# Kernel tuning notes

Measured on AMD Instinct MI355X. Metric: run time of the kernel, lower is better.

The kernel has to match this reference:

```python
import jax, jax.numpy as jnp
import numpy as np

N_EMBED = 2048
N_HEAD = 16
HEAD_DIM = N_EMBED // N_HEAD
ROPE_BASE = 500000


def _rope_cos_sin(T, dim, base):
    # torchtune RotaryPositionalEmbeddings: interleaved pairs
    inv_freq = 1.0 / (base ** (jnp.arange(0, dim, 2, dtype=jnp.float32) / dim))  # [dim/2]
    pos = jnp.arange(T, dtype=jnp.float32)
    ang = pos[:, None] * inv_freq[None, :]  # [T, dim/2]
    return jnp.cos(ang), jnp.sin(ang)


def _apply_rope(x, cos, sin):
    # x: [B, T, H, D]; cos/sin: [T, D/2] -> broadcast [1, T, 1, D/2]
    c = cos[None, :, None, :]
    s = sin[None, :, None, :]
    x1 = x[..., 0::2]
    x2 = x[..., 1::2]
    r1 = x1 * c - x2 * s
    r2 = x2 * c + x1 * s
    return jnp.stack([r1, r2], axis=-1).reshape(x.shape)


def setup_inputs() -> dict:
    key = jax.random.key(0)
    k1, k2, k3 = jax.random.split(key, 3)
    B, T, C = 4, 2048, N_EMBED
    x = jax.random.normal(k1, (B, T, C), dtype=jnp.float32)
    Wqkv = jax.random.normal(k2, (C, 3 * C), dtype=jnp.float32) * 0.02
    Wproj = jax.random.normal(k3, (C, C), dtype=jnp.float32) * 0.02
    return {"x": x, "Wqkv": Wqkv, "Wproj": Wproj}


def reference(x, Wqkv, Wproj):
    B, T, C = x.shape
    H, D = N_HEAD, HEAD_DIM
    qkv = x @ Wqkv  # [B, T, 3C]
    q, k, v = jnp.split(qkv, 3, axis=2)
    q = q.reshape(B, T, H, D)
    k = k.reshape(B, T, H, D)
    v = v.reshape(B, T, H, D)
    cos, sin = _rope_cos_sin(T, D, ROPE_BASE)
    q = _apply_rope(q, cos, sin)
    k = _apply_rope(k, cos, sin)
    scale = 1.0 / jnp.sqrt(jnp.float32(D))
    # causal SDPA: scores [B, H, T, T]
    scores = jnp.einsum('bqhd,bkhd->bhqk', q, k) * scale
    mask = jnp.tril(jnp.ones((T, T), dtype=bool))
    scores = jnp.where(mask[None, None, :, :], scores, jnp.float32(-1e30))
    attn = jax.nn.softmax(scores, axis=-1)
    y = jnp.einsum('bhqk,bkhd->bqhd', attn, v).reshape(B, T, C)
    return y @ Wproj
```

## Files before the change

### kernel.cpp

```cpp
#include <hip/hip_runtime.h>
#include <math.h>

#define NB 4
#define TT 2048
#define CC 2048
#define HH 16
#define DD 128
#define N3 6144
#define MM 8192
#define BH 64

typedef short bf8 __attribute__((ext_vector_type(8)));
typedef float f32x4 __attribute__((ext_vector_type(4)));
typedef unsigned short u16x8 __attribute__((ext_vector_type(8)));
typedef unsigned short u16;

constexpr float SCALE_QK  = 0.08838834764831843f;
constexpr float NEG_ALPHA = -0.20503692777194262f;

__device__ __forceinline__ u16 f2bf(float x) {
    unsigned int u = __float_as_uint(x);
    u += 0x7fffu + ((u >> 16) & 1u);
    return (u16)(u >> 16);
}
__device__ __forceinline__ float bf2f(u16 h) { return __uint_as_float(((unsigned int)h) << 16); }

__device__ __forceinline__ void gl_lds16(const u16* g, u16* l) {
    __builtin_amdgcn_global_load_lds(reinterpret_cast<const unsigned int*>(g),
                                     reinterpret_cast<unsigned int*>(l), 16, 0, 0);
}
__device__ __forceinline__ f32x4 MFMA(bf8 a, bf8 b, f32x4 c) {
    return __builtin_amdgcn_mfma_f32_16x16x32_bf16(a, b, c, 0, 0, 0);
}

#define BAR()    __builtin_amdgcn_s_barrier()
#define SCHED0() __builtin_amdgcn_sched_barrier(0)
#define WAIT_LGKM0() do { asm volatile("s_waitcnt lgkmcnt(0)" ::: "memory"); SCHED0(); } while (0)
#define WAIT_VM8()   do { asm volatile("s_waitcnt vmcnt(8)"   ::: "memory"); SCHED0(); } while (0)
#define WAIT_VM4()   do { asm volatile("s_waitcnt vmcnt(4)"   ::: "memory"); SCHED0(); } while (0)
#define WAIT_VM0()   do { asm volatile("s_waitcnt vmcnt(0)"   ::: "memory"); SCHED0(); } while (0)

__global__ void rope_tab_k(float* __restrict__ tab) {
    int t = blockIdx.x, p = threadIdx.x;
    float inv = expf((float)p * NEG_ALPHA);
    float s, c;
    sincosf((float)t * inv, &s, &c);
    tab[(t * 64 + p) * 2]     = c;
    tab[(t * 64 + p) * 2 + 1] = s;
}

__global__ __launch_bounds__(256) void split_x_k(const float* __restrict__ X,
                                                 u16* __restrict__ H, u16* __restrict__ L) {
    size_t base = ((size_t)blockIdx.x * 256 + threadIdx.x) * 16;
    #pragma unroll
    for (int g = 0; g < 2; ++g) {
        u16x8 hv, lv;
        #pragma unroll
        for (int j = 0; j < 8; j += 4) {
            float4 a = *(const float4*)(X + base + g * 8 + j);
            float xs[4] = {a.x, a.y, a.z, a.w};
            #pragma unroll
            for (int q = 0; q < 4; ++q) {
                u16 h = f2bf(xs[q]);
                hv[j + q] = h;
                lv[j + q] = f2bf(xs[q] - bf2f(h));
            }
        }
        *(u16x8*)&H[base + g * 8] = hv;
        *(u16x8*)&L[base + g * 8] = lv;
    }
}

__global__ __launch_bounds__(256) void splitT_h(const float* __restrict__ W,
                                                u16* __restrict__ OH,
                                                int Kd, int Nd) {
    __shared__ float tile[64][68];
    int k0 = blockIdx.x * 64, n0 = blockIdx.y * 64;
    {
        int r = threadIdx.x >> 2, cg = threadIdx.x & 3;
        const float* src = W + (size_t)(k0 + r) * Nd + n0 + cg * 16;
        #pragma unroll
        for (int j = 0; j < 4; ++j)
            *(float4*)&tile[r][cg * 16 + j * 4] = *(const float4*)(src + j * 4);
    }
    __syncthreads();
    int nl = threadIdx.x >> 2, kg = threadIdx.x & 3;
    u16x8 hv[2];
    #pragma unroll
    for (int j = 0; j < 16; ++j)
        hv[j >> 3][j & 7] = f2bf(tile[kg * 16 + j][nl]);
    size_t off = (size_t)(n0 + nl) * Kd + k0 + kg * 16;
    *(u16x8*)&OH[off]     = hv[0];
    *(u16x8*)&OH[off + 8] = hv[1];
}

template<int MODE>
__global__ __launch_bounds__(512, 2) void gemm8p(
    const u16* __restrict__ Ahp, const u16* __restrict__ Alp,
    const u16* __restrict__ Bhp,
    u16* __restrict__ Qh, u16* __restrict__ Ql,
    u16* __restrict__ Kbo, u16* __restrict__ Vto,
    const float* __restrict__ tab, float* __restrict__ Out)
{
    __shared__ u16 SM[66048];

    const int tid = threadIdx.x;
    const int w = tid >> 6, ln = tid & 63;
    const int lo4 = ln & 15, hi4 = ln >> 4;
    const int wr = w >> 2, wc = w & 3;
    const int m0 = blockIdx.x * 256, n0 = blockIdx.y * 256;
    const int NKT = 64;

    f32x4 acc[8][4];
    #pragma unroll
    for (int i = 0; i < 8; ++i)
        #pragma unroll
        for (int j = 0; j < 4; ++j) acc[i][j] = (f32x4){0.f, 0.f, 0.f, 0.f};

    auto stage = [&](int s) {
        if (s >= 4 * NKT) return;
        const int tau = s >> 2, j = s & 3;
        const int c2 = tau & 1, op = j >> 1, hf = j & 1;
        const int tdiv = tau >> 5, tmod = tau & 31;
        const u16* plane;
        int row0;
        if (op == 0) { plane = tdiv ? Alp : Ahp; row0 = m0 + hf * 128; }
        else         { plane = Bhp;              row0 = n0 + hf * 128; }
        u16* dst = SM + (op ? 32768 : 0) + (c2 * 2 + hf) * 8192;
        #pragma unroll
        for (int i = 0; i < 2; ++i) {
            int L = i * 8192 + tid * 16;
            int r = L >> 7;
            int c = (L >> 4) & 7;
            int cs = c ^ (r & 7);
            gl_lds16(plane + (size_t)(row0 + r) * 2048 + tmod * 64 + cs * 8,
                     dst + (L >> 1));
        }
    };

    #pragma unroll
    for (int s = 0; s < 6; ++s) stage(s);
    WAIT_VM4();
    BAR();

    bf8 a03[4][2], a47[4][2], b01[2][2], b23[2][2];
    const int brow0 = (wc & 1) * 64;

    for (int t = 0; t < NKT; ++t) {
        const int c2 = t & 1;
        const u16* Ab = SM + (c2 * 2 + wr) * 8192;
        const u16* Bb = SM + 32768 + (c2 * 2 + (wc >> 1)) * 8192;

        #pragma unroll
        for (int mf = 0; mf < 4; ++mf) {
            int rr = mf * 16 + lo4, s7 = rr & 7;
            a03[mf][0] = *(const bf8*)&Ab[rr * 64 + ((hi4 ^ s7)) * 8];
            a03[mf][1] = *(const bf8*)&Ab[rr * 64 + (((4 + hi4) ^ s7)) * 8];
        }
        #pragma unroll
        for (int nf = 0; nf < 2; ++nf) {
            int rr = brow0 + nf * 16 + lo4, s7 = rr & 7;
            b01[nf][0] = *(const bf8*)&Bb[rr * 64 + ((hi4 ^ s7)) * 8];
            b01[nf][1] = *(const bf8*)&Bb[rr * 64 + (((4 + hi4) ^ s7)) * 8];
        }
        stage(4 * t + 6);
        BAR(); WAIT_LGKM0();
        __builtin_amdgcn_s_setprio(1);
        #pragma unroll
        for (int mf = 0; mf < 4; ++mf)
            #pragma unroll
            for (int nf = 0; nf < 2; ++nf) {
                acc[mf][nf] = MFMA(a03[mf][0], b01[nf][0], acc[mf][nf]);
                acc[mf][nf] = MFMA(a03[mf][1], b01[nf][1], acc[mf][nf]);
            }
        __builtin_amdgcn_s_setprio(0);
        BAR();

        #pragma unroll
        for (int mf = 0; mf < 4; ++mf) {
            int rr = 64 + mf * 16 + lo4, s7 = rr & 7;
            a47[mf][0] = *(const bf8*)&Ab[rr * 64 + ((hi4 ^ s7)) * 8];
            a47[mf][1] = *(const bf8*)&Ab[rr * 64 + (((4 + hi4) ^ s7)) * 8];
        }
        stage(4 * t + 7);
        BAR(); WAIT_LGKM0();
        __builtin_amdgcn_s_setprio(1);
        #pragma unroll
        for (int mf = 0; mf < 4; ++mf)
            #pragma unroll
            for (int nf = 0; nf < 2; ++nf) {
                acc[4 + mf][nf] = MFMA(a47[mf][0], b01[nf][0], acc[4 + mf][nf]);
                acc[4 + mf][nf] = MFMA(a47[mf][1], b01[nf][1], acc[4 + mf][nf]);
            }
        __builtin_amdgcn_s_setprio(0);
        BAR();

        #pragma unroll
        for (int nf = 0; nf < 2; ++nf) {
            int rr = brow0 + 32 + nf * 16 + lo4, s7 = rr & 7;
            b23[nf][0] = *(const bf8*)&Bb[rr * 64 + ((hi4 ^ s7)) * 8];
            b23[nf][1] = *(const bf8*)&Bb[rr * 64 + (((4 + hi4) ^ s7)) * 8];
        }
        stage(4 * t + 8);
        BAR(); WAIT_LGKM0();
        __builtin_amdgcn_s_setprio(1);
        #pragma unroll
        for (int mf = 0; mf < 4; ++mf)
            #pragma unroll
            for (int nf = 0; nf < 2; ++nf) {
                acc[mf][2 + nf] = MFMA(a03[mf][0], b23[nf][0], acc[mf][2 + nf]);
                acc[mf][2 + nf] = MFMA(a03[mf][1], b23[nf][1], acc[mf][2 + nf]);
            }
        __builtin_amdgcn_s_setprio(0);
        BAR();

        stage(4 * t + 9);
        BAR();
        __builtin_amdgcn_s_setprio(1);
        #pragma unroll
        for (int mf = 0; mf < 4; ++mf)
            #pragma unroll
            for (int nf = 0; nf < 2; ++nf) {
                acc[4 + mf][2 + nf] = MFMA(a47[mf][0], b23[nf][0], acc[4 + mf][2 + nf]);
                acc[4 + mf][2 + nf] = MFMA(a47[mf][1], b23[nf][1], acc[4 + mf][2 + nf]);
            }
        __builtin_amdgcn_s_setprio(0);
        if (t < NKT - 2)       { WAIT_VM4(); }
        else if (t == NKT - 2) { WAIT_VM0(); }
        BAR();
    }

    if (MODE == 1) {
        #pragma unroll
        for (int mf = 0; mf < 8; ++mf)
            #pragma unroll
            for (int r = 0; r < 4; ++r) {
                int m = m0 + wr * 128 + mf * 16 + hi4 * 4 + r;
                float* rowp = Out + (size_t)m * CC + n0 + wc * 64;
                #pragma unroll
                for (int nf = 0; nf < 4; ++nf)
                    rowp[nf * 16 + lo4] = acc[mf][nf][r];
            }
        return;
    }

    const int sec = n0 >> 11;
    const int hh0 = (n0 >> 7) & 15;
    if (sec < 2) {
        #pragma unroll
        for (int mf = 0; mf < 8; ++mf)
            #pragma unroll
            for (int r = 0; r < 4; ++r) {
                int m = m0 + wr * 128 + mf * 16 + hi4 * 4 + r;
                int t = m & 2047, b = m >> 11;
                #pragma unroll
                for (int nf = 0; nf < 4; ++nf) {
                    int nl = wc * 64 + nf * 16 + lo4;
                    int h = hh0 + (nl >> 7), d = nl & 127;
                    float v = acc[mf][nf][r];
                    float o = __shfl_xor(v, 1);
                    const float2 cs2 = *(const float2*)&tab[(((size_t)t << 6) + (d >> 1)) * 2];
                    float rv = (ln & 1) ? (v * cs2.x + o * cs2.y)
                                        : (v * cs2.x - o * cs2.y);
                    size_t off = (((size_t)(b * HH + h)) * TT + t) * DD + d;
                    if (sec == 0) {
                        rv *= SCALE_QK;
                        u16 hv = f2bf(rv);
                        Qh[off] = hv;
                        Ql[off] = f2bf(rv - bf2f(hv));
                    } else {
                        Kbo[off] = f2bf(rv);
                    }
                }
            }
    } else {
        BAR();
        #pragma unroll
        for (int mf = 0; mf < 8; ++mf)
            #pragma unroll
            for (int r = 0; r < 4; ++r) {
                int tl = wr * 128 + mf * 16 + hi4 * 4 + r;
                #pragma unroll
                for (int nf = 0; nf < 4; ++nf) {
                    int nl = wc * 64 + nf * 16 + lo4;
                    SM[tl * 258 + nl] = f2bf(acc[mf][nf][r]);
                }
            }
        BAR();
        int nl = tid >> 1, th = tid & 1;
        int head = hh0 + (nl >> 7), d = nl & 127;
        int b = m0 >> 11, t0 = m0 & 2047;
        size_t base = (((size_t)(b * HH + head)) * DD + d) * TT + t0 + th * 128;
        #pragma unroll
        for (int g = 0; g < 16; ++g) {
            u16x8 vv;
            #pragma unroll
            for (int j = 0; j < 8; ++j) vv[j] = SM[(th * 128 + g * 8 + j) * 258 + nl];
            *(u16x8*)&Vto[base + g * 8] = vv;
        }
    }
}

__global__ __launch_bounds__(256, 2) void attn128(
    const u16* __restrict__ Qhp, const u16* __restrict__ Qlp,
    const u16* __restrict__ Kb,  const u16* __restrict__ Vt,
    u16* __restrict__ Yh, u16* __restrict__ Yl)
{
    __shared__ u16 SM[40960];

    const int tid = threadIdx.x;
    const int w = tid >> 6, ln = tid & 63;
    const int lo4 = ln & 15, hi4 = ln >> 4;
    const int bx = blockIdx.x;
    const int qt = (bx & 1) ? (15 - (bx >> 1)) : (bx >> 1);
    const int bh = blockIdx.y;
    const int q0 = qt * 128;
    const int last = 2 * qt + 1;

    const size_t qoff = ((size_t)bh * TT + q0) * DD;
    #pragma unroll
    for (int i = 0; i < 8; ++i) {
        int L = i * 4096 + tid * 16;
        int r = L >> 8, c = (L >> 4) & 15;
        int cs = c ^ (r & 7);
        gl_lds16(Qhp + qoff + r * DD + cs * 8, &SM[L >> 1]);
        gl_lds16(Qlp + qoff + r * DD + cs * 8, &SM[16384 + (L >> 1)]);
    }
    WAIT_VM0();
    BAR();
    bf8 qh[2][4], ql[2][4];
    #pragma unroll
    for (int mf = 0; mf < 2; ++mf) {
        int rq = w * 32 + mf * 16 + lo4, s7 = rq & 7;
        #pragma unroll
        for (int ks = 0; ks < 4; ++ks) {
            int ch = (ks * 4 + hi4) ^ s7;
            qh[mf][ks] = *(const bf8*)&SM[rq * 128 + ch * 8];
            ql[mf][ks] = *(const bf8*)&SM[16384 + rq * 128 + ch * 8];
        }
    }
    WAIT_LGKM0();
    BAR();

    auto stageKV = [&](int kt2, int buf) {
        const size_t koff = ((size_t)bh * TT + kt2 * 64) * DD;
        u16* kd = &SM[buf * 8192];
        #pragma unroll
        for (int i = 0; i < 4; ++i) {
            int L = i * 4096 + tid * 16;
            int r = L >> 8, c = (L >> 4) & 15, cs = c ^ (r & 7);
            gl_lds16(Kb + koff + r * DD + cs * 8, kd + (L >> 1));
        }
        const size_t voff = (size_t)bh * DD * TT + (size_t)kt2 * 64;
        u16* vd = &SM[16384 + buf * 8192];
        #pragma unroll
        for (int i = 0; i < 4; ++i) {
            int L = i * 4096 + tid * 16;
            int r = L >> 7, c = (L >> 4) & 7, cs = c ^ (r & 7);
            gl_lds16(Vt + voff + (size_t)r * TT + cs * 8, vd + (L >> 1));
        }
    };
    stageKV(0, 0);

    f32x4 O[2][8];
    #pragma unroll
    for (int mf = 0; mf < 2; ++mf)
        #pragma unroll
        for (int i = 0; i < 8; ++i) O[mf][i] = (f32x4){0.f, 0.f, 0.f, 0.f};
    float m_r[2][4], l_r[2][4];
    #pragma unroll
    for (int mf = 0; mf < 2; ++mf)
        #pragma unroll
        for (int r = 0; r < 4; ++r) { m_r[mf][r] = -1e30f; l_r[mf][r] = 0.f; }

    for (int kt = 0; kt <= last; ++kt) {
        const int cur = kt & 1;
        if (kt < last) { stageKV(kt + 1, cur ^ 1); WAIT_VM8(); }
        else           { WAIT_VM0(); }
        BAR();
        const u16* Kcur = &SM[cur * 8192];
        const u16* Vcur = &SM[16384 + cur * 8192];

        f32x4 sf[2][4];
        #pragma unroll
        for (int nf = 0; nf < 4; ++nf) {
            f32x4 s0 = (f32x4){0.f, 0.f, 0.f, 0.f};
            f32x4 s1 = (f32x4){0.f, 0.f, 0.f, 0.f};
            int kr = nf * 16 + lo4, s7 = kr & 7;
            #pragma unroll
            for (int ks = 0; ks < 4; ++ks) {
                bf8 bb = *(const bf8*)&Kcur[kr * 128 + ((ks * 4 + hi4) ^ s7) * 8];
                s0 = MFMA(qh[0][ks], bb, s0);
                s0 = MFMA(ql[0][ks], bb, s0);
                s1 = MFMA(qh[1][ks], bb, s1);
                s1 = MFMA(ql[1][ks], bb, s1);
            }
            sf[0][nf] = s0; sf[1][nf] = s1;
        }
        if (kt >= 2 * qt) {
            #pragma unroll
            for (int mf = 0; mf < 2; ++mf)
                #pragma unroll
                for (int nf = 0; nf < 4; ++nf)
                    #pragma unroll
                    for (int r = 0; r < 4; ++r) {
                        int kg = kt * 64 + nf * 16 + lo4;
                        int qg = q0 + w * 32 + mf * 16 + hi4 * 4 + r;
                        if (kg > qg) sf[mf][nf][r] = -1e30f;
                    }
        }

        #pragma unroll
        for (int mf = 0; mf < 2; ++mf) {
            float mx[4];
            #pragma unroll
            for (int r = 0; r < 4; ++r) {
                float m2 = fmaxf(fmaxf(sf[mf][0][r], sf[mf][1][r]),
                                 fmaxf(sf[mf][2][r], sf[mf][3][r]));
                m2 = fmaxf(m2, __shfl_xor(m2, 1));
                m2 = fmaxf(m2, __shfl_xor(m2, 2));
                m2 = fmaxf(m2, __shfl_xor(m2, 4));
                m2 = fmaxf(m2, __shfl_xor(m2, 8));
                mx[r] = m2;
            }
            float al[4] = {1.f, 1.f, 1.f, 1.f};
            bool grow = (mx[0] > m_r[mf][0]) || (mx[1] > m_r[mf][1]) ||
                        (mx[2] > m_r[mf][2]) || (mx[3] > m_r[mf][3]);
            if (__any(grow)) {
                #pragma unroll
                for (int r = 0; r < 4; ++r) {
                    float mn = fmaxf(m_r[mf][r], mx[r]);
                    al[r] = __expf(m_r[mf][r] - mn);
                    m_r[mf][r] = mn;
                }
                #pragma unroll
                for (int nf2 = 0; nf2 < 8; ++nf2)
                    #pragma unroll
                    for (int r = 0; r < 4; ++r) O[mf][nf2][r] *= al[r];
            }
            #pragma unroll
            for (int r = 0; r < 4; ++r) {
                float rs = 0.f;
                #pragma unroll
                for (int nf = 0; nf < 4; ++nf) {
                    float p = __expf(sf[mf][nf][r] - m_r[mf][r]);
                    sf[mf][nf][r] = p;
                    rs += p;
                }
                rs += __shfl_xor(rs, 1);
                rs += __shfl_xor(rs, 2);
                rs += __shfl_xor(rs, 4);
                rs += __shfl_xor(rs, 8);
                l_r[mf][r] = l_r[mf][r] * al[r] + rs;
            }
        }

        u16* pw = &SM[32768 + w * 2048];
        #pragma unroll
        for (int mf = 0; mf < 2; ++mf)
            #pragma unroll
            for (int r = 0; r < 4; ++r) {
                int row = mf * 16 + hi4 * 4 + r;
                int sw = (row & 7) << 3;
                #pragma unroll
                for (int nf = 0; nf < 4; ++nf)
                    pw[row * 64 + ((nf * 16 + lo4) ^ sw)] = f2bf(sf[mf][nf][r]);
            }
        bf8 pa[2][2];
        #pragma unroll
        for (int mf = 0; mf < 2; ++mf) {
            int rp = mf * 16 + lo4, s3 = rp & 7;
            pa[mf][0] = *(const bf8*)&pw[rp * 64 + ((hi4 ^ s3) * 8)];
            pa[mf][1] = *(const bf8*)&pw[rp * 64 + (((4 + hi4) ^ s3) * 8)];
        }
        #pragma unroll
        for (int nf2 = 0; nf2 < 8; ++nf2) {
            int vr = nf2 * 16 + lo4, s7 = vr & 7;
            #pragma unroll
            for (int ks = 0; ks < 2; ++ks) {
                bf8 vb = *(const bf8*)&Vcur[vr * 64 + ((ks * 4 + hi4) ^ s7) * 8];
                O[0][nf2] = MFMA(pa[0][ks], vb, O[0][nf2]);
                O[1][nf2] = MFMA(pa[1][ks], vb, O[1][nf2]);
            }
        }
        BAR();
    }

    const int b = bh >> 4, h = bh & 15;
    #pragma unroll
    for (int mf = 0; mf < 2; ++mf)
        #pragma unroll
        for (int r = 0; r < 4; ++r) {
            float inv = 1.0f / l_r[mf][r];
            int t = q0 + w * 32 + mf * 16 + hi4 * 4 + r;
            size_t rowo = ((size_t)(b * TT + t)) * CC + h * DD;
            #pragma unroll
            for (int nf2 = 0; nf2 < 8; ++nf2) {
                float val = O[mf][nf2][r] * inv;
                u16 hv = f2bf(val);
                Yh[rowo + nf2 * 16 + lo4] = hv;
                Yl[rowo + nf2 * 16 + lo4] = f2bf(val - bf2f(hv));
            }
        }
}

extern "C" void kernel_launch(void* const* d_in, const int* in_sizes, int n_in,
                              void* d_out, int out_size, void* d_ws, size_t ws_size,
                              hipStream_t stream)
{
    const float* X     = (const float*)d_in[0];
    const float* Wqkv  = (const float*)d_in[1];
    const float* Wproj = (const float*)d_in[2];

    char* W = (char*)d_ws;
    float* tab = (float*)W;
    u16* Wqh = (u16*)(W + (1u << 20));
    u16* Wph = Wqh + 12582912;
    u16* Xh  = Wph + 4194304;
    u16* Xl  = Xh + 16777216;
    u16* Kb  = Xl + 16777216;
    u16* Vt  = Kb + 16777216;

    u16* Qh = (u16*)d_out;
    u16* Ql = Qh + 16777216;

    u16* Yh = Xh;
    u16* Yl = Xl;

    rope_tab_k<<<dim3(2048), 64, 0, stream>>>(tab);
    split_x_k<<<dim3(4096), 256, 0, stream>>>(X, Xh, Xl);
    splitT_h<<<dim3(32, 96), 256, 0, stream>>>(Wqkv, Wqh, 2048, 6144);
    splitT_h<<<dim3(32, 32), 256, 0, stream>>>(Wproj, Wph, 2048, 2048);

    gemm8p<0><<<dim3(32, 24), 512, 0, stream>>>(Xh, Xl, Wqh,
                                                Qh, Ql, Kb, Vt, tab, nullptr);
    attn128<<<dim3(16, 64), 256, 0, stream>>>(Qh, Ql, Kb, Vt, Yh, Yl);
    gemm8p<1><<<dim3(32, 8), 512, 0, stream>>>(Yh, Yl, Wph,
                                               nullptr, nullptr, nullptr, nullptr,
                                               nullptr, (float*)d_out);
}
```

Measured before the change: 1.017 ms.

## Switch GEMMs to 32x32x16 MFMA tiles and remap block order for XCD locality

Replaces the 16x16x32 bf16 MFMA fragments in the QKV and projection GEMMs with 32x32x16 MFMA, so each wave issues fewer, larger matrix instructions and does fewer LDS fragment reads per output. The epilogues are rewritten for the 32x32 accumulator register layout. The grid is also flattened to 1D with a block-id swizzle, (bid&7)*N + bid>>3, which groups neighbouring tiles onto the same XCD to improve L2 reuse. The cost is more accumulator registers per fragment and a different epilogue access pattern.

```diff
diff --git a/kernel.cpp b/kernel.cpp
--- a/kernel.cpp
+++ b/kernel.cpp
@@ -12,6 +12,7 @@
 
 typedef short bf8 __attribute__((ext_vector_type(8)));
 typedef float f32x4 __attribute__((ext_vector_type(4)));
+typedef float f32x16 __attribute__((ext_vector_type(16)));
 typedef unsigned short u16x8 __attribute__((ext_vector_type(8)));
 typedef unsigned short u16;
 
@@ -31,6 +32,9 @@
 }
 __device__ __forceinline__ f32x4 MFMA(bf8 a, bf8 b, f32x4 c) {
     return __builtin_amdgcn_mfma_f32_16x16x32_bf16(a, b, c, 0, 0, 0);
+}
+__device__ __forceinline__ f32x16 MFMA32(bf8 a, bf8 b, f32x16 c) {
+    return __builtin_amdgcn_mfma_f32_32x32x16_bf16(a, b, c, 0, 0, 0);
 }
 
 #define BAR()    __builtin_amdgcn_s_barrier()
@@ -95,27 +99,30 @@
 }
 
 template<int MODE>
-__global__ __launch_bounds__(512, 2) void gemm8p(
+__device__ __forceinline__ void gemm32_body(
     const u16* __restrict__ Ahp, const u16* __restrict__ Alp,
     const u16* __restrict__ Bhp,
     u16* __restrict__ Qh, u16* __restrict__ Ql,
     u16* __restrict__ Kbo, u16* __restrict__ Vto,
-    const float* __restrict__ tab, float* __restrict__ Out)
+    const float* __restrict__ tab, float* __restrict__ Out,
+    int bx, int by)
 {
     __shared__ u16 SM[66048];
 
     const int tid = threadIdx.x;
     const int w = tid >> 6, ln = tid & 63;
-    const int lo4 = ln & 15, hi4 = ln >> 4;
+    const int l31 = ln & 31, l5 = ln >> 5;
     const int wr = w >> 2, wc = w & 3;
-    const int m0 = blockIdx.x * 256, n0 = blockIdx.y * 256;
+    const int m0 = bx * 256, n0 = by * 256;
     const int NKT = 64;
 
-    f32x4 acc[8][4];
-    #pragma unroll
-    for (int i = 0; i < 8; ++i)
-        #pragma unroll
-        for (int j = 0; j < 4; ++j) acc[i][j] = (f32x4){0.f, 0.f, 0.f, 0.f};
+    f32x16 acc[4][2];
+    #pragma unroll
+    for (int i = 0; i < 4; ++i)
+        #pragma unroll
+        for (int j = 0; j < 2; ++j)
+            #pragma unroll
+            for (int r = 0; r < 16; ++r) acc[i][j][r] = 0.f;
 
     auto stage = [&](int s) {
         if (s >= 4 * NKT) return;
@@ -143,7 +150,7 @@
     WAIT_VM4();
     BAR();
 
-    bf8 a03[4][2], a47[4][2], b01[2][2], b23[2][2];
+    bf8 aF[4][4], bF[2][4];
     const int brow0 = (wc & 1) * 64;
 
     for (int t = 0; t < NKT; ++t) {
@@ -152,65 +159,61 @@
         const u16* Bb = SM + 32768 + (c2 * 2 + (wc >> 1)) * 8192;
 
         #pragma unroll
-        for (int mf = 0; mf < 4; ++mf) {
-            int rr = mf * 16 + lo4, s7 = rr & 7;
-            a03[mf][0] = *(const bf8*)&Ab[rr * 64 + ((hi4 ^ s7)) * 8];
-            a03[mf][1] = *(const bf8*)&Ab[rr * 64 + (((4 + hi4) ^ s7)) * 8];
-        }
-        #pragma unroll
-        for (int nf = 0; nf < 2; ++nf) {
-            int rr = brow0 + nf * 16 + lo4, s7 = rr & 7;
-            b01[nf][0] = *(const bf8*)&Bb[rr * 64 + ((hi4 ^ s7)) * 8];
-            b01[nf][1] = *(const bf8*)&Bb[rr * 64 + (((4 + hi4) ^ s7)) * 8];
+        for (int mt = 0; mt < 2; ++mt) {
+            int rl = mt * 32 + l31, s7 = rl & 7;
+            #pragma unroll
+            for (int ks = 0; ks < 4; ++ks)
+                aF[mt][ks] = *(const bf8*)&Ab[rl * 64 + (((ks * 2 + l5) ^ s7)) * 8];
+        }
+        {
+            int rl = brow0 + l31, s7 = rl & 7;
+            #pragma unroll
+            for (int ks = 0; ks < 4; ++ks)
+                bF[0][ks] = *(const bf8*)&Bb[rl * 64 + (((ks * 2 + l5) ^ s7)) * 8];
         }
         stage(4 * t + 6);
         BAR(); WAIT_LGKM0();
         __builtin_amdgcn_s_setprio(1);
         #pragma unroll
-        for (int mf = 0; mf < 4; ++mf)
-            #pragma unroll
-            for (int nf = 0; nf < 2; ++nf) {
-                acc[mf][nf] = MFMA(a03[mf][0], b01[nf][0], acc[mf][nf]);
-                acc[mf][nf] = MFMA(a03[mf][1], b01[nf][1], acc[mf][nf]);
-            }
+        for (int mt = 0; mt < 2; ++mt)
+            #pragma unroll
+            for (int ks = 0; ks < 4; ++ks)
+                acc[mt][0] = MFMA32(aF[mt][ks], bF[0][ks], acc[mt][0]);
         __builtin_amdgcn_s_setprio(0);
         BAR();
 
         #pragma unroll
-        for (int mf = 0; mf < 4; ++mf) {
-            int rr = 64 + mf * 16 + lo4, s7 = rr & 7;
-            a47[mf][0] = *(const bf8*)&Ab[rr * 64 + ((hi4 ^ s7)) * 8];
-            a47[mf][1] = *(const bf8*)&Ab[rr * 64 + (((4 + hi4) ^ s7)) * 8];
+        for (int mt = 2; mt < 4; ++mt) {
+            int rl = mt * 32 + l31, s7 = rl & 7;
+            #pragma unroll
+            for (int ks = 0; ks < 4; ++ks)
+                aF[mt][ks] = *(const bf8*)&Ab[rl * 64 + (((ks * 2 + l5) ^ s7)) * 8];
         }
         stage(4 * t + 7);
         BAR(); WAIT_LGKM0();
         __builtin_amdgcn_s_setprio(1);
         #pragma unroll
-        for (int mf = 0; mf < 4; ++mf)
-            #pragma unroll
-            for (int nf = 0; nf < 2; ++nf) {
-                acc[4 + mf][nf] = MFMA(a47[mf][0], b01[nf][0], acc[4 + mf][nf]);
-                acc[4 + mf][nf] = MFMA(a47[mf][1], b01[nf][1], acc[4 + mf][nf]);
-            }
+        for (int mt = 2; mt < 4; ++mt)
+            #pragma unroll
+            for (int ks = 0; ks < 4; ++ks)
+                acc[mt][0] = MFMA32(aF[mt][ks], bF[0][ks], acc[mt][0]);
         __builtin_amdgcn_s_setprio(0);
         BAR();
 
-        #pragma unroll
-        for (int nf = 0; nf < 2; ++nf) {
-            int rr = brow0 + 32 + nf * 16 + lo4, s7 = rr & 7;
-            b23[nf][0] = *(const bf8*)&Bb[rr * 64 + ((hi4 ^ s7)) * 8];
-            b23[nf][1] = *(const bf8*)&Bb[rr * 64 + (((4 + hi4) ^ s7)) * 8];
+        {
+            int rl = brow0 + 32 + l31, s7 = rl & 7;
+            #pragma unroll
+            for (int ks = 0; ks < 4; ++ks)
+                bF[1][ks] = *(const bf8*)&Bb[rl * 64 + (((ks * 2 + l5) ^ s7)) * 8];
         }
         stage(4 * t + 8);
         BAR(); WAIT_LGKM0();
         __builtin_amdgcn_s_setprio(1);
         #pragma unroll
-        for (int mf = 0; mf < 4; ++mf)
-            #pragma unroll
-            for (int nf = 0; nf < 2; ++nf) {
-                acc[mf][2 + nf] = MFMA(a03[mf][0], b23[nf][0], acc[mf][2 + nf]);
-                acc[mf][2 + nf] = MFMA(a03[mf][1], b23[nf][1], acc[mf][2 + nf]);
-            }
+        for (int mt = 0; mt < 2; ++mt)
+            #pragma unroll
+            for (int ks = 0; ks < 4; ++ks)
+                acc[mt][1] = MFMA32(aF[mt][ks], bF[1][ks], acc[mt][1]);
         __builtin_amdgcn_s_setprio(0);
         BAR();
 
@@ -218,28 +221,28 @@
         BAR();
         __builtin_amdgcn_s_setprio(1);
         #pragma unroll
-        for (int mf = 0; mf < 4; ++mf)
-            #pragma unroll
-            for (int nf = 0; nf < 2; ++nf) {
-                acc[4 + mf][2 + nf] = MFMA(a47[mf][0], b23[nf][0], acc[4 + mf][2 + nf]);
-                acc[4 + mf][2 + nf] = MFMA(a47[mf][1], b23[nf][1], acc[4 + mf][2 + nf]);
-            }
+        for (int mt = 2; mt < 4; ++mt)
+            #pragma unroll
+            for (int ks = 0; ks < 4; ++ks)
+                acc[mt][1] = MFMA32(aF[mt][ks], bF[1][ks], acc[mt][1]);
         __builtin_amdgcn_s_setprio(0);
         if (t < NKT - 2)       { WAIT_VM4(); }
         else if (t == NKT - 2) { WAIT_VM0(); }
         BAR();
     }
 
+    const int colbase = wc * 64 + l31;
     if (MODE == 1) {
         #pragma unroll
-        for (int mf = 0; mf < 8; ++mf)
-            #pragma unroll
-            for (int r = 0; r < 4; ++r) {
-                int m = m0 + wr * 128 + mf * 16 + hi4 * 4 + r;
-                float* rowp = Out + (size_t)m * CC + n0 + wc * 64;
-                #pragma unroll
-                for (int nf = 0; nf < 4; ++nf)
-                    rowp[nf * 16 + lo4] = acc[mf][nf][r];
+        for (int mt = 0; mt < 4; ++mt)
+            #pragma unroll
+            for (int nt = 0; nt < 2; ++nt) {
+                int n = n0 + colbase + nt * 32;
+                #pragma unroll
+                for (int reg = 0; reg < 16; ++reg) {
+                    int m = m0 + wr * 128 + mt * 32 + (reg & 3) + 8 * (reg >> 2) + 4 * l5;
+                    Out[(size_t)m * CC + n] = acc[mt][nt][reg];
+                }
             }
         return;
     }
@@ -248,16 +251,16 @@
     const int hh0 = (n0 >> 7) & 15;
     if (sec < 2) {
         #pragma unroll
-        for (int mf = 0; mf < 8; ++mf)
-            #pragma unroll
-            for (int r = 0; r < 4; ++r) {
-                int m = m0 + wr * 128 + mf * 16 + hi4 * 4 + r;
-                int t = m & 2047, b = m >> 11;
-                #pragma unroll
-                for (int nf = 0; nf < 4; ++nf) {
-                    int nl = wc * 64 + nf * 16 + lo4;
-                    int h = hh0 + (nl >> 7), d = nl & 127;
-                    float v = acc[mf][nf][r];
+        for (int mt = 0; mt < 4; ++mt)
+            #pragma unroll
+            for (int nt = 0; nt < 2; ++nt) {
+                int nl = colbase + nt * 32;
+                int h = hh0 + (nl >> 7), d = nl & 127;
+                #pragma unroll
+                for (int reg = 0; reg < 16; ++reg) {
+                    int m = m0 + wr * 128 + mt * 32 + (reg & 3) + 8 * (reg >> 2) + 4 * l5;
+                    int t = m & 2047, b = m >> 11;
+                    float v = acc[mt][nt][reg];
                     float o = __shfl_xor(v, 1);
                     const float2 cs2 = *(const float2*)&tab[(((size_t)t << 6) + (d >> 1)) * 2];
                     float rv = (ln & 1) ? (v * cs2.x + o * cs2.y)
@@ -276,14 +279,14 @@
     } else {
         BAR();
         #pragma unroll
-        for (int mf = 0; mf < 8; ++mf)
-            #pragma unroll
-            for (int r = 0; r < 4; ++r) {
-                int tl = wr * 128 + mf * 16 + hi4 * 4 + r;
-                #pragma unroll
-                for (int nf = 0; nf < 4; ++nf) {
-                    int nl = wc * 64 + nf * 16 + lo4;
-                    SM[tl * 258 + nl] = f2bf(acc[mf][nf][r]);
+        for (int mt = 0; mt < 4; ++mt)
+            #pragma unroll
+            for (int nt = 0; nt < 2; ++nt) {
+                int nl = colbase + nt * 32;
+                #pragma unroll
+                for (int reg = 0; reg < 16; ++reg) {
+                    int tl = wr * 128 + mt * 32 + (reg & 3) + 8 * (reg >> 2) + 4 * l5;
+                    SM[tl * 258 + nl] = f2bf(acc[mt][nt][reg]);
                 }
             }
         BAR();
@@ -299,6 +302,28 @@
             *(u16x8*)&Vto[base + g * 8] = vv;
         }
     }
+}
+
+__global__ __launch_bounds__(512, 2) void qkv_gemm32(
+    const u16* __restrict__ Ahp, const u16* __restrict__ Alp,
+    const u16* __restrict__ Bhp,
+    u16* __restrict__ Qh, u16* __restrict__ Ql,
+    u16* __restrict__ Kbo, u16* __restrict__ Vto,
+    const float* __restrict__ tab)
+{
+    int bid = blockIdx.x;
+    int wg = (bid & 7) * 96 + (bid >> 3);
+    gemm32_body<0>(Ahp, Alp, Bhp, Qh, Ql, Kbo, Vto, tab, nullptr,
+                   wg & 31, wg >> 5);
+}
+__global__ __launch_bounds__(512, 2) void proj_gemm32(
+    const u16* __restrict__ Ahp, const u16* __restrict__ Alp,
+    const u16* __restrict__ Bhp, float* __restrict__ Out)
+{
+    int bid = blockIdx.x;
+    int wg = (bid & 7) * 32 + (bid >> 3);
+    gemm32_body<1>(Ahp, Alp, Bhp, nullptr, nullptr, nullptr, nullptr,
+                   nullptr, Out, wg & 31, wg >> 5);
 }
 
 __global__ __launch_bounds__(256, 2) void attn128(
@@ -532,10 +557,7 @@
     splitT_h<<<dim3(32, 96), 256, 0, stream>>>(Wqkv, Wqh, 2048, 6144);
     splitT_h<<<dim3(32, 32), 256, 0, stream>>>(Wproj, Wph, 2048, 2048);
 
-    gemm8p<0><<<dim3(32, 24), 512, 0, stream>>>(Xh, Xl, Wqh,
-                                                Qh, Ql, Kb, Vt, tab, nullptr);
+    qkv_gemm32<<<dim3(768), 512, 0, stream>>>(Xh, Xl, Wqh, Qh, Ql, Kb, Vt, tab);
     attn128<<<dim3(16, 64), 256, 0, stream>>>(Qh, Ql, Kb, Vt, Yh, Yl);
-    gemm8p<1><<<dim3(32, 8), 512, 0, stream>>>(Yh, Yl, Wph,
-                                               nullptr, nullptr, nullptr, nullptr,
-                                               nullptr, (float*)d_out);
-}
+    proj_gemm32<<<dim3(256), 512, 0, stream>>>(Yh, Yl, Wph, (float*)d_out);
+}
```

Result: slower. 1.151 ms (+13.2%).
